# Performance work log

Hardware: AMD Instinct MI355X
Metric: run time of the kernel (lower is better)

## Reference

```python
import jax, jax.numpy as jnp
import numpy as np

N1 = 50000; N2 = 50000; E1 = 800000; E2 = 800000; A = 10000
D_IN = 128; NHID = 128; D_OUT = 128; RATIO = 0.5
N_SUP = int(N1 * RATIO)  # 25000 super nodes
K_HOPS = 10  # GCN(in, nhid, k=10)
NEG_INF = jnp.float32(-1e30)


def _edge_norm(src, dst, w, n):
    # symmetric degree normalization of edge weights
    deg = jax.ops.segment_sum(w, dst, num_segments=n) + 1.0
    return w * jax.lax.rsqrt(deg[src] * deg[dst])


def _prop(h, src, dst, norm, n):
    # one round of weighted message passing: h'[v] = sum_e norm_e * h[src_e]
    return jax.ops.segment_sum(norm[:, None] * h[src], dst, num_segments=n)


def _gcn_k(x, src, dst, norm, n, W, b):
    h = x @ W + b
    for _ in range(K_HOPS):
        h = _prop(h, src, dst, norm, n)
    return h


def setup_inputs() -> dict:
    key = jax.random.key(0)
    ks = jax.random.split(key, 24)
    s = 0.05
    return {
        "x": jax.random.normal(ks[0], (N1, D_IN), jnp.float32),
        "edge_index": jax.random.randint(ks[1], (2, E1), 0, N1, jnp.int32),
        "edge_weight": jax.random.uniform(ks[2], (E1,), jnp.float32),
        "y": jax.random.normal(ks[3], (N2, D_IN), jnp.float32),
        "edge_index_y": jax.random.randint(ks[4], (2, E2), 0, N2, jnp.int32),
        "edge_weight_y": jax.random.uniform(ks[5], (E2,), jnp.float32),
        "anchor_links": jax.random.randint(ks[6], (2, A), 0, N1, jnp.int32),
        "temperature": 1,
        "W_gcn": jax.random.normal(ks[7], (D_IN, NHID), jnp.float32) * s,
        "b_gcn": jnp.zeros((NHID,), jnp.float32),
        "p_score": jax.random.normal(ks[8], (NHID,), jnp.float32) * s,
        "W_conv1": jax.random.normal(ks[9], (NHID, NHID), jnp.float32) * s,
        "b_conv1": jnp.zeros((NHID,), jnp.float32),
        "W_mlp1": jax.random.normal(ks[10], (NHID, NHID), jnp.float32) * s,
        "b_mlp1": jnp.zeros((NHID,), jnp.float32),
        "W_l1": jax.random.normal(ks[11], (NHID, NHID), jnp.float32) * s,
        "W_l2": jax.random.normal(ks[12], (NHID, NHID), jnp.float32) * s,
        "W_mlp2": jax.random.normal(ks[13], (NHID, D_OUT), jnp.float32) * s,
        "b_mlp2": jnp.zeros((D_OUT,), jnp.float32),
    }


def reference(x, edge_index, edge_weight, y, edge_index_y, edge_weight_y,
              anchor_links, temperature, W_gcn, b_gcn, p_score, W_conv1,
              b_conv1, W_mlp1, b_mlp1, W_l1, W_l2, W_mlp2, b_mlp2):
    T = jnp.float32(temperature)
    src, dst = edge_index[0], edge_index[1]
    norm1 = _edge_norm(src, dst, edge_weight, N1)

    # ---- down_convs[0]: 10-hop GCN on graph 1 ----
    out_x = _gcn_k(x, src, dst, norm1, N1, W_gcn, b_gcn)  # xs[0]
    xr = jax.nn.relu(out_x)

    # ---- TransPool: score -> top-k super nodes -> attention assignment ----
    s = xr @ p_score                             # [N1]
    _, perm = jax.lax.top_k(s, N_SUP)            # original ids of super nodes
    sup_id = jnp.full((N1,), -1, jnp.int32).at[perm].set(
        jnp.arange(N_SUP, dtype=jnp.int32))
    self_ids = jnp.arange(N1, dtype=src.dtype)
    cand_node = jnp.concatenate([src, self_ids])  # node being assigned
    cand_sup = jnp.concatenate([dst, self_ids])   # candidate super node
    valid = sup_id[cand_sup] >= 0
    att = jnp.sum(xr[cand_node] * xr[cand_sup], axis=-1)
    att = att / (jnp.sqrt(jnp.float32(NHID)) * T)
    att = jnp.where(valid, att, NEG_INF)
    m = jax.ops.segment_max(att, cand_node, num_segments=N1)
    e = jnp.exp(att - m[cand_node])
    esum = jax.ops.segment_sum(e, cand_node, num_segments=N1)
    w_soft = e / esum[cand_node]                 # per-node softmax over candidates
    is_best = valid & (att >= m[cand_node])
    cluster = jnp.full((N1,), -1, jnp.int32).at[cand_node].max(
        jnp.where(is_best, sup_id[cand_sup], -1))
    has = cluster >= 0
    cluster = jnp.maximum(cluster, 0)
    match = is_best & (sup_id[cand_sup] == cluster[cand_node])
    a = jnp.zeros((N1,), jnp.float32).at[cand_node].max(
        jnp.where(match, w_soft, 0.0))
    a = jnp.where(has, a, 0.0)                   # assign_weight (P1 values)

    # coarsen: x' = P x ; A' = P A P^T via cluster relabeling
    x_pool = jax.ops.segment_sum(a[:, None] * xr, cluster, num_segments=N_SUP)
    csrc, cdst = cluster[src], cluster[dst]
    cw = edge_weight * a[src] * a[dst]

    # ---- down_convs[1]: GCNConv on coarse graph (with self loop) ----
    norm_c = _edge_norm(csrc, cdst, cw, N_SUP)
    h2 = x_pool @ W_conv1 + b_conv1
    h2 = _prop(h2, csrc, cdst, norm_c, N_SUP) + h2
    sup1 = jax.nn.relu(h2)                       # xs[1]

    # ---- MLP1 ----
    sup2 = jax.nn.relu(sup1 @ W_mlp1 + b_mlp1)

    # ---- Q = P1 @ L (sparse-sparse matmul) ----
    a1, a2 = anchor_links[0], anchor_links[1]
    anchor_w = jnp.ones((A,), jnp.float32)
    q_sup = cluster[a1]
    q_col = a2
    q_w = a[a1] * anchor_w

    # ---- graph 2: shared down_convs[0] ----
    srcy, dsty = edge_index_y[0], edge_index_y[1]
    normy = _edge_norm(srcy, dsty, edge_weight_y, N2)
    out_y = _gcn_k(y, srcy, dsty, normy, N2, W_gcn, b_gcn)

    # ---- LastLayer: Q^T (sup2 W_l1) + L^T (out_x W_l2) scattered into graph2 ----
    t1 = sup2 @ W_l1
    out_y = out_y + jax.ops.segment_sum(q_w[:, None] * t1[q_sup], q_col,
                                        num_segments=N2)
    t2 = out_x @ W_l2
    out_y = out_y + jax.ops.segment_sum(anchor_w[:, None] * t2[a1], a2,
                                        num_segments=N2)

    recon_y = out_y @ W_mlp2 + b_mlp2
    return (out_x, sup1, out_y, sup2, a, recon_y)
```

## Files before the change

### kernel.cpp

```cpp
#include <hip/hip_runtime.h>
#include <hip/hip_bf16.h>
#include <math.h>

#define N1 50000
#define N2 50000
#define E1C 800000
#define E2C 800000
#define AC 10000
#define F 128
#define NSUP 25000
#define KHOPS 10
#define NEGINF -1e30f
#define NBINS 65536
#define NBINS22 (1 << 22)

static inline int cdiv(int a, int b) { return (a + b - 1) / b; }

__device__ __forceinline__ float bf2f(unsigned short u) {
  return __uint_as_float(((unsigned)u) << 16);
}
__device__ __forceinline__ unsigned short f2bf(float f) {
  unsigned x = __float_as_uint(f);
  return (unsigned short)((x + 0x7FFFu + ((x >> 16) & 1u)) >> 16);
}

__global__ void k_count(const int* __restrict__ key, int* __restrict__ cnt, int n) {
  int e = blockIdx.x * blockDim.x + threadIdx.x;
  if (e < n) atomicAdd(&cnt[key[e]], 1);
}

__global__ void k_scan(const int* __restrict__ cnt, int* __restrict__ rowptr, int n) {
  const int T = 1024;
  int t = threadIdx.x;
  int vpt = (n + T - 1) / T;
  int lo = t * vpt, hi = lo + vpt;
  if (hi > n) hi = n;
  int sum = 0;
  for (int i = lo; i < hi; ++i) sum += cnt[i];
  int lane = t & 63, wid = t >> 6;
  int v = sum;
#pragma unroll
  for (int o = 1; o < 64; o <<= 1) {
    int u = __shfl_up(v, o, 64);
    if (lane >= o) v += u;
  }
  __shared__ int wsum[16];
  if (lane == 63) wsum[wid] = v;
  __syncthreads();
  if (t < 16) {
    int w = wsum[t];
#pragma unroll
    for (int o = 1; o < 16; o <<= 1) {
      int u = __shfl_up(w, o, 64);
      if (t >= o) w += u;
    }
    wsum[t] = w;
  }
  __syncthreads();
  int base = (wid ? wsum[wid - 1] : 0) + (v - sum);
  if (t == 0) rowptr[0] = 0;
  int run = base;
  for (int i = lo; i < hi; ++i) { run += cnt[i]; rowptr[i + 1] = run; }
}

__global__ void k_fill(const int* __restrict__ key, const int* __restrict__ payload,
                       const float* __restrict__ val, const int* __restrict__ rowptr,
                       int* __restrict__ cnt, int* __restrict__ col, float* __restrict__ v,
                       int n) {
  int e = blockIdx.x * blockDim.x + threadIdx.x;
  if (e < n) {
    int k = key[e];
    int p = atomicAdd(&cnt[k], 1);
    int s = rowptr[k] + p;
    col[s] = payload[e];
    if (val) v[s] = val[e];
  }
}

__global__ void k_fill_iota(const int* __restrict__ key, const int* __restrict__ rowptr,
                            int* __restrict__ cnt, int* __restrict__ col, int n) {
  int e = blockIdx.x * blockDim.x + threadIdx.x;
  if (e < n) {
    int k = key[e];
    int p = atomicAdd(&cnt[k], 1);
    col[rowptr[k] + p] = e;
  }
}

__global__ void k_count_coarse(const int* __restrict__ dst, const int* __restrict__ cluster,
                               int* __restrict__ cnt, int n) {
  int e = blockIdx.x * blockDim.x + threadIdx.x;
  if (e < n) atomicAdd(&cnt[cluster[dst[e]]], 1);
}

__global__ void k_fill_coarse(const int* __restrict__ src, const int* __restrict__ dst,
                              const int* __restrict__ cluster, const float* __restrict__ w,
                              const float* __restrict__ a, const int* __restrict__ rowptr,
                              int* __restrict__ cnt, int* __restrict__ col,
                              float* __restrict__ v, int n) {
  int e = blockIdx.x * blockDim.x + threadIdx.x;
  if (e < n) {
    int sd = dst[e];
    int k = cluster[sd];
    int p = atomicAdd(&cnt[k], 1);
    int s = rowptr[k] + p;
    int ss = src[e];
    col[s] = cluster[ss];
    v[s] = w[e] * a[ss] * a[sd];
  }
}

__global__ void k_rowsum(const int* __restrict__ rowptr, const float* __restrict__ v,
                         float* __restrict__ deg, int n) {
  int row = blockIdx.x * 8 + (threadIdx.x >> 5);
  if (row >= n) return;
  int q = threadIdx.x & 31;
  int s0 = rowptr[row], s1 = rowptr[row + 1];
  float s = 0.f;
  for (int k = s0 + q; k < s1; k += 32) s += v[k];
#pragma unroll
  for (int o = 16; o; o >>= 1) s += __shfl_xor(s, o, 64);
  if (q == 0) deg[row] = s;
}

__global__ void k_csrnorm(const int* __restrict__ rowptr, const int* __restrict__ col,
                          float* __restrict__ v, const float* __restrict__ deg, int n) {
  int row = blockIdx.x * 8 + (threadIdx.x >> 5);
  if (row >= n) return;
  int q = threadIdx.x & 31;
  int s0 = rowptr[row], s1 = rowptr[row + 1];
  float di = deg[row] + 1.f;
  for (int s = s0 + q; s < s1; s += 32) {
    float dc = deg[col[s]] + 1.f;
    v[s] = v[s] / sqrtf(dc * di);
  }
}

__global__ void k_prop(const float4* __restrict__ hin, float4* __restrict__ hout,
                       float4* __restrict__ relu_out, const int* __restrict__ rowptr,
                       const int* __restrict__ col, const float* __restrict__ val, int n) {
  int node = blockIdx.x * 8 + (threadIdx.x >> 5);
  if (node >= n) return;
  int q = threadIdx.x & 31;
  int grp = threadIdx.x & 32;
  int s0 = rowptr[node], s1 = rowptr[node + 1];
  float4 acc = make_float4(0.f, 0.f, 0.f, 0.f);
  for (int s = s0; s < s1; s += 32) {
    int es = s + q;
    int ok = es < s1;
    int sc = ok ? es : (s1 - 1);
    int cme = col[sc];
    float vme = ok ? val[sc] : 0.f;
    int nb = s1 - s; if (nb > 32) nb = 32;
    for (int j = 0; j < nb; j += 8) {
      int c8[8]; float v8[8];
#pragma unroll
      for (int t = 0; t < 8; ++t) {
        c8[t] = __shfl(cme, grp + j + t, 64);
        v8[t] = __shfl(vme, grp + j + t, 64);
      }
      float4 h[8];
#pragma unroll
      for (int t = 0; t < 8; ++t) h[t] = hin[(size_t)c8[t] * 32 + q];
#pragma unroll
      for (int t = 0; t < 8; ++t) {
        acc.x = fmaf(v8[t], h[t].x, acc.x);
        acc.y = fmaf(v8[t], h[t].y, acc.y);
        acc.z = fmaf(v8[t], h[t].z, acc.z);
        acc.w = fmaf(v8[t], h[t].w, acc.w);
      }
    }
  }
  hout[(size_t)node * 32 + q] = acc;
  if (relu_out) {
    float4 r;
    r.x = fmaxf(acc.x, 0.f); r.y = fmaxf(acc.y, 0.f);
    r.z = fmaxf(acc.z, 0.f); r.w = fmaxf(acc.w, 0.f);
    relu_out[(size_t)node * 32 + q] = r;
  }
}

__global__ void k_prop_bf16(const ushort4* __restrict__ hin, ushort4* __restrict__ hout,
                            float4* __restrict__ fout, const int* __restrict__ rowptr,
                            const int* __restrict__ col, const float* __restrict__ val, int n) {
  int node = blockIdx.x * 8 + (threadIdx.x >> 5);
  if (node >= n) return;
  int q = threadIdx.x & 31;
  int grp = threadIdx.x & 32;
  int s0 = rowptr[node], s1 = rowptr[node + 1];
  float4 acc = make_float4(0.f, 0.f, 0.f, 0.f);
  for (int s = s0; s < s1; s += 32) {
    int es = s + q;
    int ok = es < s1;
    int sc = ok ? es : (s1 - 1);
    int cme = col[sc];
    float vme = ok ? val[sc] : 0.f;
    int nb = s1 - s; if (nb > 32) nb = 32;
    for (int j = 0; j < nb; j += 8) {
      int c8[8]; float v8[8];
#pragma unroll
      for (int t = 0; t < 8; ++t) {
        c8[t] = __shfl(cme, grp + j + t, 64);
        v8[t] = __shfl(vme, grp + j + t, 64);
      }
      ushort4 h[8];
#pragma unroll
      for (int t = 0; t < 8; ++t) h[t] = hin[(size_t)c8[t] * 32 + q];
#pragma unroll
      for (int t = 0; t < 8; ++t) {
        acc.x = fmaf(v8[t], bf2f(h[t].x), acc.x);
        acc.y = fmaf(v8[t], bf2f(h[t].y), acc.y);
        acc.z = fmaf(v8[t], bf2f(h[t].z), acc.z);
        acc.w = fmaf(v8[t], bf2f(h[t].w), acc.w);
      }
    }
  }
  if (fout) {
    fout[(size_t)node * 32 + q] = acc;
  } else {
    ushort4 o;
    o.x = f2bf(acc.x); o.y = f2bf(acc.y); o.z = f2bf(acc.z); o.w = f2bf(acc.w);
    hout[(size_t)node * 32 + q] = o;
  }
}

__global__ void k_transpose(const float* __restrict__ W, float* __restrict__ WT) {
  int i = blockIdx.x * blockDim.x + threadIdx.x;
  if (i < F * F) { int k = i >> 7, c = i & 127; WT[c * F + k] = W[i]; }
}

__global__ void k_mm128(const float* __restrict__ X, const float* __restrict__ WT,
                        const float* __restrict__ bias, float* __restrict__ out,
                        int M, int relu) {
  __shared__ float4 xs[16][32];
  int tid = threadIdx.x;
  int c = tid & 127;
  int half = tid >> 7;
  int row0 = blockIdx.x * 16;
  for (int t = tid; t < 512; t += 256) {
    int r = t >> 5, k4 = t & 31;
    int gr = row0 + r;
    float4 v = make_float4(0.f, 0.f, 0.f, 0.f);
    if (gr < M) v = ((const float4*)X)[(size_t)gr * 32 + k4];
    xs[r][k4] = v;
  }
  __syncthreads();
  float acc[8];
#pragma unroll
  for (int r = 0; r < 8; ++r) acc[r] = 0.f;
  const float4* wrow = (const float4*)WT + (size_t)c * 32;
  for (int k4 = 0; k4 < 32; ++k4) {
    float4 w = wrow[k4];
#pragma unroll
    for (int r = 0; r < 8; ++r) {
      float4 xv = xs[half * 8 + r][k4];
      acc[r] = fmaf(xv.x, w.x, acc[r]);
      acc[r] = fmaf(xv.y, w.y, acc[r]);
      acc[r] = fmaf(xv.z, w.z, acc[r]);
      acc[r] = fmaf(xv.w, w.w, acc[r]);
    }
  }
  float bb = bias ? bias[c] : 0.f;
#pragma unroll
  for (int r = 0; r < 8; ++r) {
    int gr = row0 + half * 8 + r;
    if (gr < M) {
      float v = acc[r] + bb;
      if (relu) v = fmaxf(v, 0.f);
      out[(size_t)gr * F + c] = v;
    }
  }
}

__global__ void k_mm128_bf16(const float* __restrict__ X, const float* __restrict__ WT,
                             const float* __restrict__ bias, unsigned short* __restrict__ out,
                             int M) {
  __shared__ float4 xs[16][32];
  int tid = threadIdx.x;
  int c = tid & 127;
  int half = tid >> 7;
  int row0 = blockIdx.x * 16;
  for (int t = tid; t < 512; t += 256) {
    int r = t >> 5, k4 = t & 31;
    int gr = row0 + r;
    float4 v = make_float4(0.f, 0.f, 0.f, 0.f);
    if (gr < M) v = ((const float4*)X)[(size_t)gr * 32 + k4];
    xs[r][k4] = v;
  }
  __syncthreads();
  float acc[8];
#pragma unroll
  for (int r = 0; r < 8; ++r) acc[r] = 0.f;
  const float4* wrow = (const float4*)WT + (size_t)c * 32;
  for (int k4 = 0; k4 < 32; ++k4) {
    float4 w = wrow[k4];
#pragma unroll
    for (int r = 0; r < 8; ++r) {
      float4 xv = xs[half * 8 + r][k4];
      acc[r] = fmaf(xv.x, w.x, acc[r]);
      acc[r] = fmaf(xv.y, w.y, acc[r]);
      acc[r] = fmaf(xv.z, w.z, acc[r]);
      acc[r] = fmaf(xv.w, w.w, acc[r]);
    }
  }
  float bb = bias ? bias[c] : 0.f;
#pragma unroll
  for (int r = 0; r < 8; ++r) {
    int gr = row0 + half * 8 + r;
    if (gr < M) out[(size_t)gr * F + c] = f2bf(acc[r] + bb);
  }
}

__global__ void k_addrelu(const float* __restrict__ a, const float* __restrict__ b,
                          float* __restrict__ out, int n) {
  int i = blockIdx.x * blockDim.x + threadIdx.x;
  if (i < n) out[i] = fmaxf(a[i] + b[i], 0.f);
}

__global__ void k_score(const float* __restrict__ xr, const float* __restrict__ p,
                        float* __restrict__ s, int n) {
  int wid = (blockIdx.x * blockDim.x + threadIdx.x) >> 6;
  int lane = threadIdx.x & 63;
  if (wid >= n) return;
  const float* row = xr + (size_t)wid * F;
  float d = row[lane] * p[lane] + row[lane + 64] * p[lane + 64];
#pragma unroll
  for (int o = 32; o; o >>= 1) d += __shfl_xor(d, o, 64);
  if (lane == 0) s[wid] = d;
}

__device__ __forceinline__ unsigned sortkey(float f) {
  if (f == 0.f) f = 0.f;
  unsigned u = __float_as_uint(f);
  return (u & 0x80000000u) ? ~u : (u | 0x80000000u);
}

__global__ void k_key(const float* __restrict__ s, unsigned* __restrict__ key, int n) {
  int i = blockIdx.x * blockDim.x + threadIdx.x;
  if (i < n) key[i] = sortkey(s[i]);
}

__global__ void k_count_bins22(const unsigned* __restrict__ key, int* __restrict__ cnt, int n) {
  int i = blockIdx.x * blockDim.x + threadIdx.x;
  if (i < n) atomicAdd(&cnt[key[i] >> 10], 1);
}

__global__ void k_hist_blocksum(const int* __restrict__ cnt, int* __restrict__ partial) {
  int t = threadIdx.x;
  int base = blockIdx.x * 1024 + t * 4;
  int s = cnt[base] + cnt[base + 1] + cnt[base + 2] + cnt[base + 3];
#pragma unroll
  for (int o = 32; o; o >>= 1) s += __shfl_down(s, o, 64);
  __shared__ int ws[4];
  int lane = t & 63, w = t >> 6;
  if (lane == 0) ws[w] = s;
  __syncthreads();
  if (t == 0) partial[blockIdx.x] = ws[0] + ws[1] + ws[2] + ws[3];
}

__global__ void k_hist_apply(const int* __restrict__ cnt, const int* __restrict__ partialptr,
                             int* __restrict__ binptr) {
  int t = threadIdx.x;
  int base = blockIdx.x * 1024 + t * 4;
  int c0 = cnt[base], c1 = cnt[base + 1], c2 = cnt[base + 2], c3 = cnt[base + 3];
  int s = c0 + c1 + c2 + c3;
  int lane = t & 63, w = t >> 6;
  int v = s;
#pragma unroll
  for (int o = 1; o < 64; o <<= 1) {
    int u = __shfl_up(v, o, 64);
    if (lane >= o) v += u;
  }
  __shared__ int ws[4];
  if (lane == 63) ws[w] = v;
  __syncthreads();
  int wb = 0;
  for (int i = 0; i < w; ++i) wb += ws[i];
  int run = partialptr[blockIdx.x] + wb + (v - s);
  binptr[base + 1] = run + c0;
  binptr[base + 2] = run + c0 + c1;
  binptr[base + 3] = run + c0 + c1 + c2;
  binptr[base + 4] = run + s;
  if (blockIdx.x == 0 && t == 0) binptr[0] = 0;
}

__global__ void k_fill_bins22(const unsigned* __restrict__ key, const int* __restrict__ binptr,
                              int* __restrict__ cnt, int* __restrict__ bidx,
                              unsigned* __restrict__ bkey, int n) {
  int i = blockIdx.x * blockDim.x + threadIdx.x;
  if (i < n) {
    unsigned k = key[i];
    int b = k >> 10;
    int p = atomicAdd(&cnt[b], 1);
    int s = binptr[b] + p;
    bidx[s] = i;
    bkey[s] = k;
  }
}

__global__ void k_rank22(const unsigned* __restrict__ key, const int* __restrict__ binptr,
                         const int* __restrict__ bidx, const unsigned* __restrict__ bkey,
                         int* __restrict__ supid, int n) {
  int i = blockIdx.x * blockDim.x + threadIdx.x;
  if (i >= n) return;
  unsigned ki = key[i];
  int b = ki >> 10;
  int cnt = n - binptr[b + 1];
  int s1 = binptr[b + 1];
  for (int s = binptr[b]; s < s1; ++s) {
    unsigned kj = bkey[s];
    cnt += (kj > ki) || (kj == ki && bidx[s] < i);
  }
  supid[i] = (cnt < NSUP) ? cnt : -1;
}

__device__ __forceinline__ float read_T(const void* p) {
  int ib = *(const int*)p;
  float fb = __int_as_float(ib);
  if (ib >= 1 && ib < (1 << 20)) return (float)ib;
  if (fb > 1e-6f && fb < 1e6f) return fb;
  return 1.0f;
}

__global__ void k_att_a(const float* __restrict__ xr, const int* __restrict__ rowptr,
                        const int* __restrict__ col, const int* __restrict__ supid,
                        const void* __restrict__ tptr, float* __restrict__ att,
                        float* __restrict__ attself, float* __restrict__ mout, int n) {
  int wid = (blockIdx.x * blockDim.x + threadIdx.x) >> 6;
  int lane = threadIdx.x & 63;
  if (wid >= n) return;
  float inv = 1.0f / (sqrtf(128.0f) * read_T(tptr));
  const float* xn = xr + (size_t)wid * F;
  float x0 = xn[lane], x1 = xn[lane + 64];
  float d = x0 * x0 + x1 * x1;
#pragma unroll
  for (int o = 32; o; o >>= 1) d += __shfl_xor(d, o, 64);
  float av = (supid[wid] >= 0) ? d * inv : NEGINF;
  float m = av;
  if (lane == 0) attself[wid] = av;
  int s0 = rowptr[wid], s1 = rowptr[wid + 1];
  for (int s = s0; s < s1; s += 4) {
    int c[4]; bool ok[4];
#pragma unroll
    for (int j = 0; j < 4; ++j) {
      int ss = s + j;
      ok[j] = ss < s1;
      c[j] = col[ok[j] ? ss : (s1 - 1)];
    }
    float dd[4];
#pragma unroll
    for (int j = 0; j < 4; ++j) {
      const float* xc = xr + (size_t)c[j] * F;
      dd[j] = x0 * xc[lane] + x1 * xc[lane + 64];
    }
#pragma unroll
    for (int j = 0; j < 4; ++j) {
#pragma unroll
      for (int o = 32; o; o >>= 1) dd[j] += __shfl_xor(dd[j], o, 64);
    }
#pragma unroll
    for (int j = 0; j < 4; ++j) {
      if (ok[j]) {
        float a2 = (supid[c[j]] >= 0) ? dd[j] * inv : NEGINF;
        if (lane == 0) att[s + j] = a2;
        m = fmaxf(m, a2);
      }
    }
  }
  if (lane == 0) mout[wid] = m;
}

__global__ void k_att_b(const int* __restrict__ rowptr, const int* __restrict__ col,
                        const int* __restrict__ supid, const float* __restrict__ att,
                        const float* __restrict__ attself, const float* __restrict__ mv,
                        int* __restrict__ cluster, float* __restrict__ aout, int n) {
  int i = blockIdx.x * 8 + (threadIdx.x >> 5);
  if (i >= n) return;
  int q = threadIdx.x & 31;
  float m = mv[i];
  float as = attself[i];
  float esum = 0.f;
  int best = -1;
  if (q == 0) {
    esum = expf(as - m);
    if (as >= m) best = supid[i];
  }
  int s0 = rowptr[i], s1 = rowptr[i + 1];
  for (int s = s0 + q; s < s1; s += 32) {
    float av = att[s];
    esum += expf(av - m);
    if (av >= m) {
      int sid = supid[col[s]];
      if (sid > best) best = sid;
    }
  }
#pragma unroll
  for (int o = 16; o; o >>= 1) {
    esum += __shfl_xor(esum, o, 64);
    int ob = __shfl_xor(best, o, 64);
    if (ob > best) best = ob;
  }
  if (q == 0) {
    int has = best >= 0;
    cluster[i] = has ? best : 0;
    aout[i] = has ? 1.0f / esum : 0.0f;
  }
}

__global__ void k_xpool_pull(const float4* __restrict__ xr, const float* __restrict__ a,
                             const int* __restrict__ rowptrM, const int* __restrict__ memb,
                             float4* __restrict__ xpool, int n) {
  int c = blockIdx.x * 8 + (threadIdx.x >> 5);
  if (c >= n) return;
  int q = threadIdx.x & 31;
  int s0 = rowptrM[c], s1 = rowptrM[c + 1];
  float4 acc = make_float4(0.f, 0.f, 0.f, 0.f);
  for (int s = s0; s < s1; ++s) {
    int m = memb[s];
    float av = a[m];
    float4 h = xr[(size_t)m * 32 + q];
    acc.x = fmaf(av, h.x, acc.x);
    acc.y = fmaf(av, h.y, acc.y);
    acc.z = fmaf(av, h.z, acc.z);
    acc.w = fmaf(av, h.w, acc.w);
  }
  xpool[(size_t)c * 32 + q] = acc;
}

__global__ void k_scatter_q(const int* __restrict__ a1, const int* __restrict__ a2,
                            const int* __restrict__ cluster, const float* __restrict__ aarr,
                            const float* __restrict__ t1, float* __restrict__ outy, int nA) {
  int idx = blockIdx.x * blockDim.x + threadIdx.x;
  if (idx >= nA * F) return;
  int k = idx >> 7, f = idx & 127;
  int n1 = a1[k];
  float qw = aarr[n1];
  if (qw != 0.f)
    atomicAdd(&outy[(size_t)a2[k] * F + f], qw * t1[(size_t)cluster[n1] * F + f]);
}

__global__ void k_scatter_t2(const int* __restrict__ a1, const int* __restrict__ a2,
                             const float* __restrict__ t2, float* __restrict__ outy, int nA) {
  int idx = blockIdx.x * blockDim.x + threadIdx.x;
  if (idx >= nA * F) return;
  int k = idx >> 7, f = idx & 127;
  atomicAdd(&outy[(size_t)a2[k] * F + f], t2[(size_t)a1[k] * F + f]);
}

extern "C" void kernel_launch(void* const* d_in, const int* in_sizes, int n_in,
                              void* d_out, int out_size, void* d_ws, size_t ws_size,
                              hipStream_t stream) {
  (void)in_sizes; (void)n_in; (void)out_size; (void)ws_size;
  const float* x   = (const float*)d_in[0];
  const int*   ei  = (const int*)d_in[1];
  const float* w1  = (const float*)d_in[2];
  const float* y   = (const float*)d_in[3];
  const int*   eiy = (const int*)d_in[4];
  const float* wy  = (const float*)d_in[5];
  const int*   anc = (const int*)d_in[6];
  const void*  tmp = d_in[7];
  const float* W_gcn = (const float*)d_in[8];
  const float* b_gcn = (const float*)d_in[9];
  const float* p_sc  = (const float*)d_in[10];
  const float* W_c1  = (const float*)d_in[11];
  const float* b_c1  = (const float*)d_in[12];
  const float* W_m1  = (const float*)d_in[13];
  const float* b_m1  = (const float*)d_in[14];
  const float* W_l1  = (const float*)d_in[15];
  const float* W_l2  = (const float*)d_in[16];
  const float* W_m2  = (const float*)d_in[17];
  const float* b_m2  = (const float*)d_in[18];

  float* out   = (float*)d_out;
  float* out_x = out;
  float* sup1  = out_x + (size_t)N1 * F;
  float* out_y = sup1 + (size_t)NSUP * F;
  float* sup2  = out_y + (size_t)N2 * F;
  float* a_out = sup2 + (size_t)NSUP * F;
  float* recon = a_out + N1;

  char* wsb = (char*)d_ws;
  size_t off = 0;
  auto alloc = [&](size_t bytes) -> void* {
    void* p = wsb + off;
    off = (off + bytes + 255) & ~(size_t)255;
    return p;
  };
  float*    f_csr1v   = (float*)alloc((size_t)E1C * 4);
  int*      i_csr1c   = (int*)alloc((size_t)E1C * 4);
  int*      i_rowptr1 = (int*)alloc((size_t)(N1 + 1) * 4);
  float*    f_deg     = (float*)alloc((size_t)N1 * 4);
  int*      i_cnt     = (int*)alloc((size_t)(NBINS + 1) * 4);
  float*    f_ha      = (float*)alloc((size_t)N1 * F * 4);
  float*    f_hb      = (float*)alloc((size_t)N1 * F * 4);
  float*    f_xr      = (float*)alloc((size_t)N1 * F * 4);
  float*    f_s       = (float*)alloc((size_t)N1 * 4);
  unsigned* u_key     = (unsigned*)alloc((size_t)N1 * 4);
  int*      i_partial = (int*)alloc((size_t)4096 * 4);
  int*      i_partptr = (int*)alloc((size_t)4097 * 4);
  int*      i_bidx    = (int*)alloc((size_t)N1 * 4);
  unsigned* u_bkey    = (unsigned*)alloc((size_t)N1 * 4);
  int*      i_supid   = (int*)alloc((size_t)N1 * 4);
  int*      i_rowptrS = (int*)alloc((size_t)(N1 + 1) * 4);
  int*      i_csrSc   = (int*)alloc((size_t)E1C * 4);
  float*    f_att     = (float*)alloc((size_t)E1C * 4);
  float*    f_attself = (float*)alloc((size_t)N1 * 4);
  float*    f_m       = (float*)alloc((size_t)N1 * 4);
  int*      i_cluster = (int*)alloc((size_t)N1 * 4);
  float*    f_xpool   = (float*)alloc((size_t)NSUP * F * 4);
  float*    f_degc    = (float*)alloc((size_t)NSUP * 4);
  int*      i_rowptrC = (int*)alloc((size_t)(NSUP + 1) * 4);
  int*      i_csrCc   = (int*)alloc((size_t)E1C * 4);
  float*    f_csrCv   = (float*)alloc((size_t)E1C * 4);
  int*      i_rowptrM = (int*)alloc((size_t)(NSUP + 1) * 4);
  int*      i_memb    = (int*)alloc((size_t)N1 * 4);
  float*    f_h2      = (float*)alloc((size_t)NSUP * F * 4);
  float*    f_h2p     = (float*)alloc((size_t)NSUP * F * 4);
  float*    f_wt      = (float*)alloc((size_t)6 * F * F * 4);

  int* i_cnt22    = (int*)f_ha;
  int* i_binptr22 = (int*)f_hb;
  unsigned short* h16a = (unsigned short*)f_ha;
  unsigned short* h16b = (unsigned short*)f_hb;

  const int* src1 = ei,  * dst1 = ei + E1C;
  const int* srcy = eiy, * dsty = eiy + E2C;
  const int* a1 = anc, * a2 = anc + AC;

  const float* Ws[6] = { W_gcn, W_c1, W_m1, W_l1, W_l2, W_m2 };
  for (int i = 0; i < 6; ++i)
    k_transpose<<<cdiv(F * F, 256), 256, 0, stream>>>(Ws[i], f_wt + (size_t)i * F * F);
  float* wt_gcn = f_wt, *wt_c1 = f_wt + 16384, *wt_m1 = f_wt + 2 * 16384,
       * wt_l1 = f_wt + 3 * 16384, *wt_l2 = f_wt + 4 * 16384, *wt_m2 = f_wt + 5 * 16384;

  int gE = cdiv(E1C, 256);
  int gN = cdiv(N1, 256);
  int gN8 = cdiv(N1, 8);
  int gC8 = cdiv(NSUP, 8);

  hipMemsetAsync(i_cnt, 0, (size_t)(NBINS + 1) * 4, stream);
  k_count<<<gE, 256, 0, stream>>>(dst1, i_cnt, E1C);
  k_scan<<<1, 1024, 0, stream>>>(i_cnt, i_rowptr1, N1);
  hipMemsetAsync(i_cnt, 0, (size_t)(NBINS + 1) * 4, stream);
  k_fill<<<gE, 256, 0, stream>>>(dst1, src1, w1, i_rowptr1, i_cnt, i_csr1c, f_csr1v, E1C);
  k_rowsum<<<gN8, 256, 0, stream>>>(i_rowptr1, f_csr1v, f_deg, N1);
  k_csrnorm<<<gN8, 256, 0, stream>>>(i_rowptr1, i_csr1c, f_csr1v, f_deg, N1);

  k_mm128<<<cdiv(N1, 16), 256, 0, stream>>>(x, wt_gcn, b_gcn, f_ha, N1, 0);
  {
    const float* cur = f_ha;
    for (int i = 0; i < KHOPS; ++i) {
      int last = (i == KHOPS - 1);
      float* dst = last ? out_x : ((i & 1) ? f_ha : f_hb);
      k_prop<<<gN8, 256, 0, stream>>>((const float4*)cur, (float4*)dst,
                                      last ? (float4*)f_xr : nullptr,
                                      i_rowptr1, i_csr1c, f_csr1v, N1);
      cur = dst;
    }
  }

  k_score<<<cdiv(N1, 4), 256, 0, stream>>>(f_xr, p_sc, f_s, N1);
  k_key<<<gN, 256, 0, stream>>>(f_s, u_key, N1);
  hipMemsetAsync(i_cnt22, 0, (size_t)NBINS22 * 4, stream);
  k_count_bins22<<<gN, 256, 0, stream>>>(u_key, i_cnt22, N1);
  k_hist_blocksum<<<NBINS22 / 1024, 256, 0, stream>>>(i_cnt22, i_partial);
  k_scan<<<1, 1024, 0, stream>>>(i_partial, i_partptr, 4096);
  k_hist_apply<<<NBINS22 / 1024, 256, 0, stream>>>(i_cnt22, i_partptr, i_binptr22);
  hipMemsetAsync(i_cnt22, 0, (size_t)NBINS22 * 4, stream);
  k_fill_bins22<<<gN, 256, 0, stream>>>(u_key, i_binptr22, i_cnt22, i_bidx, u_bkey, N1);
  k_rank22<<<gN, 256, 0, stream>>>(u_key, i_binptr22, i_bidx, u_bkey, i_supid, N1);

  hipMemsetAsync(i_cnt, 0, (size_t)(NBINS + 1) * 4, stream);
  k_count<<<gE, 256, 0, stream>>>(src1, i_cnt, E1C);
  k_scan<<<1, 1024, 0, stream>>>(i_cnt, i_rowptrS, N1);
  hipMemsetAsync(i_cnt, 0, (size_t)(NBINS + 1) * 4, stream);
  k_fill<<<gE, 256, 0, stream>>>(src1, dst1, (const float*)nullptr, i_rowptrS, i_cnt, i_csrSc,
                                 (float*)nullptr, E1C);

  k_att_a<<<cdiv(N1, 4), 256, 0, stream>>>(f_xr, i_rowptrS, i_csrSc, i_supid, tmp,
                                           f_att, f_attself, f_m, N1);
  k_att_b<<<gN8, 256, 0, stream>>>(i_rowptrS, i_csrSc, i_supid, f_att, f_attself,
                                   f_m, i_cluster, a_out, N1);

  hipMemsetAsync(i_cnt, 0, (size_t)(NBINS + 1) * 4, stream);
  k_count<<<gN, 256, 0, stream>>>(i_cluster, i_cnt, N1);
  k_scan<<<1, 1024, 0, stream>>>(i_cnt, i_rowptrM, NSUP);
  hipMemsetAsync(i_cnt, 0, (size_t)(NBINS + 1) * 4, stream);
  k_fill_iota<<<gN, 256, 0, stream>>>(i_cluster, i_rowptrM, i_cnt, i_memb, N1);
  k_xpool_pull<<<gC8, 256, 0, stream>>>((const float4*)f_xr, a_out, i_rowptrM,
                                        i_memb, (float4*)f_xpool, NSUP);

  hipMemsetAsync(i_cnt, 0, (size_t)(NBINS + 1) * 4, stream);
  k_count_coarse<<<gE, 256, 0, stream>>>(dst1, i_cluster, i_cnt, E1C);
  k_scan<<<1, 1024, 0, stream>>>(i_cnt, i_rowptrC, NSUP);
  hipMemsetAsync(i_cnt, 0, (size_t)(NBINS + 1) * 4, stream);
  k_fill_coarse<<<gE, 256, 0, stream>>>(src1, dst1, i_cluster, w1, a_out, i_rowptrC, i_cnt,
                                        i_csrCc, f_csrCv, E1C);
  k_rowsum<<<gC8, 256, 0, stream>>>(i_rowptrC, f_csrCv, f_degc, NSUP);
  k_csrnorm<<<gC8, 256, 0, stream>>>(i_rowptrC, i_csrCc, f_csrCv, f_degc, NSUP);

  k_mm128<<<cdiv(NSUP, 16), 256, 0, stream>>>(f_xpool, wt_c1, b_c1, f_h2, NSUP, 0);
  k_prop<<<gC8, 256, 0, stream>>>((const float4*)f_h2, (float4*)f_h2p, nullptr,
                                  i_rowptrC, i_csrCc, f_csrCv, NSUP);
  k_addrelu<<<cdiv(NSUP * F, 256), 256, 0, stream>>>(f_h2p, f_h2, sup1, NSUP * F);
  k_mm128<<<cdiv(NSUP, 16), 256, 0, stream>>>(sup1, wt_m1, b_m1, sup2, NSUP, 1);

  hipMemsetAsync(i_cnt, 0, (size_t)(NBINS + 1) * 4, stream);
  k_count<<<gE, 256, 0, stream>>>(dsty, i_cnt, E2C);
  k_scan<<<1, 1024, 0, stream>>>(i_cnt, i_rowptr1, N2);
  hipMemsetAsync(i_cnt, 0, (size_t)(NBINS + 1) * 4, stream);
  k_fill<<<gE, 256, 0, stream>>>(dsty, srcy, wy, i_rowptr1, i_cnt, i_csr1c, f_csr1v, E2C);
  k_rowsum<<<gN8, 256, 0, stream>>>(i_rowptr1, f_csr1v, f_deg, N2);
  k_csrnorm<<<gN8, 256, 0, stream>>>(i_rowptr1, i_csr1c, f_csr1v, f_deg, N2);
  k_mm128_bf16<<<cdiv(N2, 16), 256, 0, stream>>>(y, wt_gcn, b_gcn, h16a, N2);
  {
    const unsigned short* cur = h16a;
    for (int i = 0; i < KHOPS; ++i) {
      int last = (i == KHOPS - 1);
      unsigned short* dst = (i & 1) ? h16a : h16b;
      k_prop_bf16<<<gN8, 256, 0, stream>>>(
          (const ushort4*)cur, last ? nullptr : (ushort4*)dst,
          last ? (float4*)out_y : nullptr, i_rowptr1, i_csr1c, f_csr1v, N2);
      cur = dst;
    }
  }

  float* f_t1 = f_h2p;
  float* f_t2 = f_xr;
  k_mm128<<<cdiv(NSUP, 16), 256, 0, stream>>>(sup2, wt_l1, (const float*)nullptr, f_t1, NSUP, 0);
  k_scatter_q<<<cdiv(AC * F, 256), 256, 0, stream>>>(a1, a2, i_cluster, a_out, f_t1, out_y, AC);
  k_mm128<<<cdiv(N1, 16), 256, 0, stream>>>(out_x, wt_l2, (const float*)nullptr, f_t2, N1, 0);
  k_scatter_t2<<<cdiv(AC * F, 256), 256, 0, stream>>>(a1, a2, f_t2, out_y, AC);

  k_mm128<<<cdiv(N2, 16), 256, 0, stream>>>(out_y, wt_m2, b_m2, recon, N2, 0);
}
```

Baseline: 2.363 ms.

## Fuse graph-1 and graph-2 K-hop propagation into one dual kernel per hop

Graph 2's CSR build and bf16 projection now run early, right after graph 1's. Each of the 10 hops then launches a single kernel whose even blocks propagate graph 1 in fp32 and odd blocks propagate graph 2 in bf16. The aim is to halve the number of propagation launches and let the two independent gathers overlap, filling the GPU better and hiding launch and tail gaps. To make room, graph 2's CSR and bf16 buffers alias the coarse-graph and pool workspaces (i_csrCc, f_xpool, f_h2), which are only written after the loop. A separate row pointer is added for graph 2.

```diff
diff --git a/kernel.cpp b/kernel.cpp
--- a/kernel.cpp
+++ b/kernel.cpp
@@ -180,47 +180,90 @@
   }
 }
 
-__global__ void k_prop_bf16(const ushort4* __restrict__ hin, ushort4* __restrict__ hout,
-                            float4* __restrict__ fout, const int* __restrict__ rowptr,
-                            const int* __restrict__ col, const float* __restrict__ val, int n) {
-  int node = blockIdx.x * 8 + (threadIdx.x >> 5);
+__global__ void k_prop_dual(const float4* __restrict__ hin1, float4* __restrict__ hout1,
+                            float4* __restrict__ xr_out,
+                            const int* __restrict__ rp1, const int* __restrict__ col1,
+                            const float* __restrict__ val1,
+                            const ushort4* __restrict__ hin2, ushort4* __restrict__ hout2,
+                            float4* __restrict__ fout2,
+                            const int* __restrict__ rp2, const int* __restrict__ col2,
+                            const float* __restrict__ val2, int n) {
+  int node = (blockIdx.x >> 1) * 8 + (threadIdx.x >> 5);
   if (node >= n) return;
   int q = threadIdx.x & 31;
   int grp = threadIdx.x & 32;
-  int s0 = rowptr[node], s1 = rowptr[node + 1];
-  float4 acc = make_float4(0.f, 0.f, 0.f, 0.f);
-  for (int s = s0; s < s1; s += 32) {
-    int es = s + q;
-    int ok = es < s1;
-    int sc = ok ? es : (s1 - 1);
-    int cme = col[sc];
-    float vme = ok ? val[sc] : 0.f;
-    int nb = s1 - s; if (nb > 32) nb = 32;
-    for (int j = 0; j < nb; j += 8) {
-      int c8[8]; float v8[8];
-#pragma unroll
-      for (int t = 0; t < 8; ++t) {
-        c8[t] = __shfl(cme, grp + j + t, 64);
-        v8[t] = __shfl(vme, grp + j + t, 64);
+  if ((blockIdx.x & 1) == 0) {
+    int s0 = rp1[node], s1 = rp1[node + 1];
+    float4 acc = make_float4(0.f, 0.f, 0.f, 0.f);
+    for (int s = s0; s < s1; s += 32) {
+      int es = s + q;
+      int ok = es < s1;
+      int sc = ok ? es : (s1 - 1);
+      int cme = col1[sc];
+      float vme = ok ? val1[sc] : 0.f;
+      int nb = s1 - s; if (nb > 32) nb = 32;
+      for (int j = 0; j < nb; j += 8) {
+        int c8[8]; float v8[8];
+#pragma unroll
+        for (int t = 0; t < 8; ++t) {
+          c8[t] = __shfl(cme, grp + j + t, 64);
+          v8[t] = __shfl(vme, grp + j + t, 64);
+        }
+        float4 h[8];
+#pragma unroll
+        for (int t = 0; t < 8; ++t) h[t] = hin1[(size_t)c8[t] * 32 + q];
+#pragma unroll
+        for (int t = 0; t < 8; ++t) {
+          acc.x = fmaf(v8[t], h[t].x, acc.x);
+          acc.y = fmaf(v8[t], h[t].y, acc.y);
+          acc.z = fmaf(v8[t], h[t].z, acc.z);
+          acc.w = fmaf(v8[t], h[t].w, acc.w);
+        }
       }
-      ushort4 h[8];
-#pragma unroll
-      for (int t = 0; t < 8; ++t) h[t] = hin[(size_t)c8[t] * 32 + q];
-#pragma unroll
-      for (int t = 0; t < 8; ++t) {
-        acc.x = fmaf(v8[t], bf2f(h[t].x), acc.x);
-        acc.y = fmaf(v8[t], bf2f(h[t].y), acc.y);
-        acc.z = fmaf(v8[t], bf2f(h[t].z), acc.z);
-        acc.w = fmaf(v8[t], bf2f(h[t].w), acc.w);
+    }
+    hout1[(size_t)node * 32 + q] = acc;
+    if (xr_out) {
+      float4 r;
+      r.x = fmaxf(acc.x, 0.f); r.y = fmaxf(acc.y, 0.f);
+      r.z = fmaxf(acc.z, 0.f); r.w = fmaxf(acc.w, 0.f);
+      xr_out[(size_t)node * 32 + q] = r;
+    }
+  } else {
+    int s0 = rp2[node], s1 = rp2[node + 1];
+    float4 acc = make_float4(0.f, 0.f, 0.f, 0.f);
+    for (int s = s0; s < s1; s += 32) {
+      int es = s + q;
+      int ok = es < s1;
+      int sc = ok ? es : (s1 - 1);
+      int cme = col2[sc];
+      float vme = ok ? val2[sc] : 0.f;
+      int nb = s1 - s; if (nb > 32) nb = 32;
+      for (int j = 0; j < nb; j += 8) {
+        int c8[8]; float v8[8];
+#pragma unroll
+        for (int t = 0; t < 8; ++t) {
+          c8[t] = __shfl(cme, grp + j + t, 64);
+          v8[t] = __shfl(vme, grp + j + t, 64);
+        }
+        ushort4 h[8];
+#pragma unroll
+        for (int t = 0; t < 8; ++t) h[t] = hin2[(size_t)c8[t] * 32 + q];
+#pragma unroll
+        for (int t = 0; t < 8; ++t) {
+          acc.x = fmaf(v8[t], bf2f(h[t].x), acc.x);
+          acc.y = fmaf(v8[t], bf2f(h[t].y), acc.y);
+          acc.z = fmaf(v8[t], bf2f(h[t].z), acc.z);
+          acc.w = fmaf(v8[t], bf2f(h[t].w), acc.w);
+        }
       }
     }
-  }
-  if (fout) {
-    fout[(size_t)node * 32 + q] = acc;
-  } else {
-    ushort4 o;
-    o.x = f2bf(acc.x); o.y = f2bf(acc.y); o.z = f2bf(acc.z); o.w = f2bf(acc.w);
-    hout[(size_t)node * 32 + q] = o;
+    if (fout2) {
+      fout2[(size_t)node * 32 + q] = acc;
+    } else {
+      ushort4 o;
+      o.x = f2bf(acc.x); o.y = f2bf(acc.y); o.z = f2bf(acc.z); o.w = f2bf(acc.w);
+      hout2[(size_t)node * 32 + q] = o;
+    }
   }
 }
 
@@ -589,6 +632,7 @@
   float*    f_csr1v   = (float*)alloc((size_t)E1C * 4);
   int*      i_csr1c   = (int*)alloc((size_t)E1C * 4);
   int*      i_rowptr1 = (int*)alloc((size_t)(N1 + 1) * 4);
+  int*      i_rowptr2 = (int*)alloc((size_t)(N2 + 1) * 4);
   float*    f_deg     = (float*)alloc((size_t)N1 * 4);
   int*      i_cnt     = (int*)alloc((size_t)(NBINS + 1) * 4);
   float*    f_ha      = (float*)alloc((size_t)N1 * F * 4);
@@ -620,8 +664,10 @@
 
   int* i_cnt22    = (int*)f_ha;
   int* i_binptr22 = (int*)f_hb;
-  unsigned short* h16a = (unsigned short*)f_ha;
-  unsigned short* h16b = (unsigned short*)f_hb;
+  int*   i_csr2c  = i_csrCc;
+  float* f_csr2v  = f_csrCv;
+  unsigned short* h16a = (unsigned short*)f_xpool;
+  unsigned short* h16b = (unsigned short*)f_h2;
 
   const int* src1 = ei,  * dst1 = ei + E1C;
   const int* srcy = eiy, * dsty = eiy + E2C;
@@ -637,6 +683,7 @@
   int gN = cdiv(N1, 256);
   int gN8 = cdiv(N1, 8);
   int gC8 = cdiv(NSUP, 8);
+  int gD = 2 * cdiv(N1, 8);
 
   hipMemsetAsync(i_cnt, 0, (size_t)(NBINS + 1) * 4, stream);
   k_count<<<gE, 256, 0, stream>>>(dst1, i_cnt, E1C);
@@ -646,16 +693,30 @@
   k_rowsum<<<gN8, 256, 0, stream>>>(i_rowptr1, f_csr1v, f_deg, N1);
   k_csrnorm<<<gN8, 256, 0, stream>>>(i_rowptr1, i_csr1c, f_csr1v, f_deg, N1);
 
+  hipMemsetAsync(i_cnt, 0, (size_t)(NBINS + 1) * 4, stream);
+  k_count<<<gE, 256, 0, stream>>>(dsty, i_cnt, E2C);
+  k_scan<<<1, 1024, 0, stream>>>(i_cnt, i_rowptr2, N2);
+  hipMemsetAsync(i_cnt, 0, (size_t)(NBINS + 1) * 4, stream);
+  k_fill<<<gE, 256, 0, stream>>>(dsty, srcy, wy, i_rowptr2, i_cnt, i_csr2c, f_csr2v, E2C);
+  k_rowsum<<<gN8, 256, 0, stream>>>(i_rowptr2, f_csr2v, f_deg, N2);
+  k_csrnorm<<<gN8, 256, 0, stream>>>(i_rowptr2, i_csr2c, f_csr2v, f_deg, N2);
+
   k_mm128<<<cdiv(N1, 16), 256, 0, stream>>>(x, wt_gcn, b_gcn, f_ha, N1, 0);
+  k_mm128_bf16<<<cdiv(N2, 16), 256, 0, stream>>>(y, wt_gcn, b_gcn, h16a, N2);
+
   {
-    const float* cur = f_ha;
+    const float* cur1 = f_ha;
+    const unsigned short* cur2 = h16a;
     for (int i = 0; i < KHOPS; ++i) {
       int last = (i == KHOPS - 1);
-      float* dst = last ? out_x : ((i & 1) ? f_ha : f_hb);
-      k_prop<<<gN8, 256, 0, stream>>>((const float4*)cur, (float4*)dst,
-                                      last ? (float4*)f_xr : nullptr,
-                                      i_rowptr1, i_csr1c, f_csr1v, N1);
-      cur = dst;
+      float* dst1b = last ? out_x : ((i & 1) ? f_ha : f_hb);
+      unsigned short* dst2b = (i & 1) ? h16a : h16b;
+      k_prop_dual<<<gD, 256, 0, stream>>>(
+          (const float4*)cur1, (float4*)dst1b, last ? (float4*)f_xr : nullptr,
+          i_rowptr1, i_csr1c, f_csr1v,
+          (const ushort4*)cur2, (ushort4*)dst2b, last ? (float4*)out_y : nullptr,
+          i_rowptr2, i_csr2c, f_csr2v, N1);
+      cur1 = dst1b; cur2 = dst2b;
     }
   }
 
@@ -705,26 +766,6 @@
   k_addrelu<<<cdiv(NSUP * F, 256), 256, 0, stream>>>(f_h2p, f_h2, sup1, NSUP * F);
   k_mm128<<<cdiv(NSUP, 16), 256, 0, stream>>>(sup1, wt_m1, b_m1, sup2, NSUP, 1);
 
-  hipMemsetAsync(i_cnt, 0, (size_t)(NBINS + 1) * 4, stream);
-  k_count<<<gE, 256, 0, stream>>>(dsty, i_cnt, E2C);
-  k_scan<<<1, 1024, 0, stream>>>(i_cnt, i_rowptr1, N2);
-  hipMemsetAsync(i_cnt, 0, (size_t)(NBINS + 1) * 4, stream);
-  k_fill<<<gE, 256, 0, stream>>>(dsty, srcy, wy, i_rowptr1, i_cnt, i_csr1c, f_csr1v, E2C);
-  k_rowsum<<<gN8, 256, 0, stream>>>(i_rowptr1, f_csr1v, f_deg, N2);
-  k_csrnorm<<<gN8, 256, 0, stream>>>(i_rowptr1, i_csr1c, f_csr1v, f_deg, N2);
-  k_mm128_bf16<<<cdiv(N2, 16), 256, 0, stream>>>(y, wt_gcn, b_gcn, h16a, N2);
-  {
-    const unsigned short* cur = h16a;
-    for (int i = 0; i < KHOPS; ++i) {
-      int last = (i == KHOPS - 1);
-      unsigned short* dst = (i & 1) ? h16a : h16b;
-      k_prop_bf16<<<gN8, 256, 0, stream>>>(
-          (const ushort4*)cur, last ? nullptr : (ushort4*)dst,
-          last ? (float4*)out_y : nullptr, i_rowptr1, i_csr1c, f_csr1v, N2);
-      cur = dst;
-    }
-  }
-
   float* f_t1 = f_h2p;
   float* f_t2 = f_xr;
   k_mm128<<<cdiv(NSUP, 16), 256, 0, stream>>>(sup2, wt_l1, (const float*)nullptr, f_t1, NSUP, 0);
```

Measured after the change: 2.357 ms. About the same (-0.3%).
